# Kernel tuning notes

Hardware: AMD Instinct MI355X
Metric: run time of the kernel (lower is better)

## Reference

```python
import jax, jax.numpy as jnp
import numpy as np

B, S, D, H = 4, 2048, 1024, 4
HD = D // H


def setup_inputs() -> dict:
    key = jax.random.key(0)
    ks = jax.random.split(key, 6)
    s = 0.02  # init scale for projection weights
    return {
        "hidden_states": jax.random.normal(ks[0], (B, S, D), jnp.float32),
        "Wq": jax.random.normal(ks[1], (D, D), jnp.float32) * s,
        "Wk": jax.random.normal(ks[2], (D, D), jnp.float32) * s,
        "Wv": jax.random.normal(ks[3], (D, D), jnp.float32) * s,
        "Wo": jax.random.normal(ks[4], (D, D), jnp.float32) * s,
        "bo": jnp.zeros((D,), jnp.float32),
        "betas": jax.random.normal(ks[5], (1, H, 1, 1), jnp.float32),
        "mem": jnp.zeros((H, HD, HD), jnp.float32),
        "z": jnp.zeros((H, HD, 1), jnp.float32),
    }


def reference(hidden_states, Wq, Wk, Wv, Wo, bo, betas, mem, z):
    b, s, d = hidden_states.shape
    h = betas.shape[1]
    hd = d // h

    def split(x):  # [b,s,d] -> [b,h,s,hd]
        return x.reshape(b, s, h, hd).transpose(0, 2, 1, 3)

    q = split(hidden_states @ Wq.T)
    k = split(hidden_states @ Wk.T)
    v = split(hidden_states @ Wv.T)

    # standard causal attention (note: no 1/sqrt(d) scaling, faithful to source)
    aw = jnp.einsum('bhqd,bhkd->bhqk', q, k)
    causal = jnp.tril(jnp.ones((s, s), bool))
    aw = jnp.where(causal, aw, jnp.finfo(aw.dtype).min)
    p = jax.nn.softmax(aw, axis=-1)
    attn = jnp.einsum('bhqk,bhkd->bhqd', p, v)

    # linear-attention memory read
    sq = jax.nn.elu(q) + 1.0
    sk = jax.nn.elu(k) + 1.0
    A_mem = jnp.einsum('bhsd,hde->bhse', sq, mem) / (
        jnp.einsum('bhsd,hdo->bhso', sq, z) + 1e-6)

    # sigmoid-gated blend
    g = jax.nn.sigmoid(betas)
    out = g * A_mem + (1.0 - g) * attn

    # memory / z state update (delta rule), averaged over batch
    delta = jnp.einsum('bhsd,hde->bhse', sk, mem) / (
        jnp.einsum('bhsd,hdo->bhso', sk, z) + 1e-6)
    mem_new = mem + jnp.einsum('bhsd,bhse->hde', sk, v - delta) / b
    z_new = z + jnp.mean(jnp.sum(sk, axis=2), axis=0)[:, :, None]

    # merge heads + output projection
    out = out.transpose(0, 2, 1, 3).reshape(b, s, d)
    out = out @ Wo.T + bo
    return (out, mem_new, z_new)
```

## Files before the change

kernel.cpp:

```cpp
#include <hip/hip_runtime.h>

#define Bsz 4
#define Ssz 2048
#define Dsz 1024
#define Hsz 4
#define HDsz 256
#define Msz 8192

typedef unsigned short u16;
typedef __attribute__((ext_vector_type(8))) short bf16x8;
typedef __attribute__((ext_vector_type(4))) float f32x4;

__device__ __forceinline__ u16 f2b(float f) {
  unsigned u = __float_as_uint(f);
  return (u16)((u + 0x7FFFu + ((u >> 16) & 1u)) >> 16);
}
__device__ __forceinline__ unsigned pk2(float a, float b) {
  return (unsigned)f2b(a) | ((unsigned)f2b(b) << 16);
}

typedef const unsigned int __attribute__((address_space(1)))* gcp;
typedef unsigned int __attribute__((address_space(3)))* lcp;
__device__ __forceinline__ void gld16(const u16* g, u16* l) {
  __builtin_amdgcn_global_load_lds((gcp)g, (lcp)l, 16, 0, 0);
}

__global__ __launch_bounds__(256) void cvt_bf16(const float4* __restrict__ in,
                                                u16* __restrict__ outp) {
  size_t i = (size_t)blockIdx.x * 256 + threadIdx.x;
  float4 v = in[i];
  uint2 r; r.x = pk2(v.x, v.y); r.y = pk2(v.z, v.w);
  *(uint2*)(outp + i * 4) = r;
}

__global__ __launch_bounds__(256) void gemm_lds(const u16* __restrict__ A16,
                                                const u16* __restrict__ Wb,
                                                const float* __restrict__ bias,
                                                float* __restrict__ C32,
                                                u16* __restrict__ Cbf) {
  __shared__ u16 sA[128 * 32];
  __shared__ u16 sB[128 * 32];
  const int tid = threadIdx.x;
  const int lane = tid & 63, quad = lane >> 4, l15 = lane & 15;
  const int w = tid >> 6;
  const int mw = (w >> 1) * 64, nw = (w & 1) * 64;
  const int m0 = blockIdx.y * 128, n0 = blockIdx.x * 128;
  const int r0 = tid >> 2, seg = (tid & 3) * 8;
  const u16* ga0 = A16 + (size_t)(m0 + r0) * Dsz + seg;
  const u16* gb0 = Wb + (size_t)(n0 + r0) * Dsz + seg;
  u16* lA0 = sA + w * 512;
  u16* lA1 = sA + 2048 + w * 512;
  u16* lB0 = sB + w * 512;
  u16* lB1 = sB + 2048 + w * 512;
  f32x4 acc[4][4] = {};
  for (int k0 = 0; k0 < Dsz; k0 += 32) {
    __syncthreads();
    gld16(ga0 + k0, lA0);
    gld16(ga0 + (size_t)64 * Dsz + k0, lA1);
    gld16(gb0 + k0, lB0);
    gld16(gb0 + (size_t)64 * Dsz + k0, lB1);
    __syncthreads();
    bf16x8 af[4], bfr[4];
#pragma unroll
    for (int i = 0; i < 4; ++i) {
      af[i] = *(const bf16x8*)&sA[(mw + i * 16 + l15) * 32 + quad * 8];
      bfr[i] = *(const bf16x8*)&sB[(nw + i * 16 + l15) * 32 + quad * 8];
    }
#pragma unroll
    for (int i = 0; i < 4; ++i)
#pragma unroll
      for (int j = 0; j < 4; ++j)
        acc[i][j] = __builtin_amdgcn_mfma_f32_16x16x32_bf16(af[i], bfr[j], acc[i][j], 0, 0, 0);
  }
#pragma unroll
  for (int j = 0; j < 4; ++j) {
    const int n = n0 + nw + j * 16 + l15;
    const float bv = bias ? bias[n] : 0.f;
#pragma unroll
    for (int i = 0; i < 4; ++i) {
#pragma unroll
      for (int r = 0; r < 4; ++r) {
        const int m = m0 + mw + i * 16 + quad * 4 + r;
        const float val = acc[i][j][r] + bv;
        const size_t idx = (size_t)m * Dsz + n;
        if (C32) C32[idx] = val;
        if (Cbf) Cbf[idx] = f2b(val);
      }
    }
  }
}

__global__ __launch_bounds__(256) void transpose_v(const float* __restrict__ V,
                                                   u16* __restrict__ Vt) {
  __shared__ u16 tile[32 * 36];
  const int t = threadIdx.x;
  const int s0 = blockIdx.x * 32, e0 = blockIdx.y * 32, bh = blockIdx.z;
  const int b = bh >> 2, h = bh & 3;
  {
    const int s_l = t >> 3, e8 = (t & 7) * 4;
    float4 v = *(const float4*)(V + ((size_t)(b * Ssz) + s0 + s_l) * Dsz + h * HDsz + e0 + e8);
    uint2 r; r.x = pk2(v.x, v.y); r.y = pk2(v.z, v.w);
    *(uint2*)&tile[s_l * 36 + e8] = r;
  }
  __syncthreads();
  {
    const int e_l = t >> 3, s4 = (t & 7) * 4;
    u16 a = tile[(s4 + 0) * 36 + e_l], b2 = tile[(s4 + 1) * 36 + e_l];
    u16 c = tile[(s4 + 2) * 36 + e_l], d = tile[(s4 + 3) * 36 + e_l];
    uint2 r; r.x = (unsigned)a | ((unsigned)b2 << 16);
    r.y = (unsigned)c | ((unsigned)d << 16);
    *(uint2*)(Vt + ((size_t)bh * HDsz + e0 + e_l) * Ssz + s0 + s4) = r;
  }
}

__global__ __launch_bounds__(256, 2) void attn_mfma(const u16* __restrict__ Qg,
                                                    const u16* __restrict__ Kg,
                                                    const u16* __restrict__ Vtg,
                                                    float* __restrict__ At,
                                                    float* __restrict__ Pb,
                                                    float* __restrict__ mlb) {
  const int x = blockIdx.x;
  int qt, cc; bool split;
  if (x < 40) { qt = 31 - (x >> 1); cc = x & 1; split = true; }
  else { qt = 51 - x; cc = 0; split = false; }
  const int bh = blockIdx.y, b = bh >> 2, h = bh & 3;
  const int tid = threadIdx.x, w = tid >> 6, lane = tid & 63;
  const int quad = lane >> 4, l15 = lane & 15;
  __shared__ u16 sK[2][32 * 256];
  __shared__ u16 sV[2][256 * 32];
  const int q0w = qt * 64 + w * 16;
  bf16x8 qf[8];
  {
    const u16* qp = Qg + ((size_t)(b * Ssz) + q0w + l15) * Dsz + h * HDsz + quad * 8;
#pragma unroll
    for (int dd = 0; dd < 8; ++dd) qf[dd] = *(const bf16x8*)(qp + dd * 32);
  }
  f32x4 o[16] = {};
  float m_old = -1e30f, l = 0.f;
  const int nkt = 2 * qt + 2, half = qt + 1;
  const int kt_lo = (split && cc) ? half : 0;
  const int kt_hi = (split && !cc) ? half : nkt;
  const u16* kstage = Kg + ((size_t)(b * Ssz) + (tid >> 5)) * Dsz + h * HDsz
                      + (((tid & 31) ^ ((tid >> 5) & 7)) << 3);
  const u16* vstage = Vtg + ((size_t)bh * HDsz + (tid >> 2)) * Ssz
                      + (((tid & 3) ^ ((tid >> 3) & 3)) << 3);
  int bufc = 0;
  {
    const u16* kp = kstage + (size_t)(kt_lo * 32) * Dsz;
    const u16* vp = vstage + kt_lo * 32;
#pragma unroll
    for (int i = 0; i < 4; ++i) {
      gld16(kp + (size_t)i * 8 * Dsz, &sK[0][w * 512 + i * 2048]);
      gld16(vp + (size_t)i * 64 * Ssz, &sV[0][w * 512 + i * 2048]);
    }
  }
  for (int kt = kt_lo; kt < kt_hi; ++kt) {
    const int j0 = kt * 32;
    __syncthreads();
    if (kt + 1 < kt_hi) {
      const u16* kp = kstage + (size_t)((kt + 1) * 32) * Dsz;
      const u16* vp = vstage + (kt + 1) * 32;
      const int bn = bufc ^ 1;
#pragma unroll
      for (int i = 0; i < 4; ++i) {
        gld16(kp + (size_t)i * 8 * Dsz, &sK[bn][w * 512 + i * 2048]);
        gld16(vp + (size_t)i * 64 * Ssz, &sV[bn][w * 512 + i * 2048]);
      }
    }
    f32x4 s0v = {}, s1v = {};
#pragma unroll
    for (int dd = 0; dd < 8; ++dd) {
      const int c0 = ((dd * 4 + quad) ^ (l15 & 7)) << 3;
      bf16x8 a0 = *(const bf16x8*)&sK[bufc][l15 * 256 + c0];
      bf16x8 a1 = *(const bf16x8*)&sK[bufc][(16 + l15) * 256 + c0];
      s0v = __builtin_amdgcn_mfma_f32_16x16x32_bf16(a0, qf[dd], s0v, 0, 0, 0);
      s1v = __builtin_amdgcn_mfma_f32_16x16x32_bf16(a1, qf[dd], s1v, 0, 0, 0);
    }
    const int qg = q0w + l15;
    float p[8];
#pragma unroll
    for (int r = 0; r < 4; ++r) {
      const int kg = j0 + quad * 4 + r;
      p[r] = (kg <= qg) ? s0v[r] : -1e30f;
      p[4 + r] = (kg + 16 <= qg) ? s1v[r] : -1e30f;
    }
    float mt = p[0];
#pragma unroll
    for (int i = 1; i < 8; ++i) mt = fmaxf(mt, p[i]);
    mt = fmaxf(mt, __shfl_xor(mt, 16));
    mt = fmaxf(mt, __shfl_xor(mt, 32));
    const float m_new = fmaxf(m_old, mt);
    const float alpha = __expf(m_old - m_new);
    float ts = 0.f;
#pragma unroll
    for (int i = 0; i < 8; ++i) { p[i] = __expf(p[i] - m_new); ts += p[i]; }
    ts += __shfl_xor(ts, 16);
    ts += __shfl_xor(ts, 32);
    l = l * alpha + ts;
    m_old = m_new;
    if (!__all(alpha == 1.0f)) {
      const float a0_ = __shfl(alpha, (lane & 48) | (quad * 4 + 0));
      const float a1_ = __shfl(alpha, (lane & 48) | (quad * 4 + 1));
      const float a2_ = __shfl(alpha, (lane & 48) | (quad * 4 + 2));
      const float a3_ = __shfl(alpha, (lane & 48) | (quad * 4 + 3));
#pragma unroll
      for (int ds = 0; ds < 16; ++ds) {
        o[ds][0] *= a0_; o[ds][1] *= a1_; o[ds][2] *= a2_; o[ds][3] *= a3_;
      }
    }
    float xx[8];
#pragma unroll
    for (int i = 0; i < 8; ++i) xx[i] = __shfl_xor(p[i], 16);
    const bool qe = (quad & 1) == 0;
    float Alo[8], Ahi[8];
#pragma unroll
    for (int i = 0; i < 4; ++i) {
      Alo[i] = qe ? p[i] : xx[i];
      Alo[4 + i] = qe ? xx[i] : p[i];
      Ahi[i] = qe ? p[4 + i] : xx[4 + i];
      Ahi[4 + i] = qe ? xx[4 + i] : p[4 + i];
    }
    float zz[8];
    const bool sendlo = (quad & 1) != 0;
#pragma unroll
    for (int i = 0; i < 8; ++i) zz[i] = __shfl_xor(sendlo ? Alo[i] : Ahi[i], 32);
    float fin[8];
#pragma unroll
    for (int i = 0; i < 8; ++i)
      fin[i] = (quad == 0) ? Alo[i] : (quad == 3) ? Ahi[i] : zz[i];
    uint4 pkv;
    pkv.x = pk2(fin[0], fin[1]); pkv.y = pk2(fin[2], fin[3]);
    pkv.z = pk2(fin[4], fin[5]); pkv.w = pk2(fin[6], fin[7]);
    bf16x8 pf = *(bf16x8*)&pkv;
    const int vc0 = (quad ^ ((l15 >> 1) & 3)) << 3;
#pragma unroll
    for (int ds = 0; ds < 16; ++ds) {
      bf16x8 bv = *(const bf16x8*)&sV[bufc][(ds * 16 + l15) * 32 + vc0];
      o[ds] = __builtin_amdgcn_mfma_f32_16x16x32_bf16(pf, bv, o[ds], 0, 0, 0);
    }
    bufc ^= 1;
  }
  if (!split) {
    float lr[4];
#pragma unroll
    for (int r = 0; r < 4; ++r) lr[r] = 1.f / __shfl(l, (lane & 48) | (quad * 4 + r));
    float* ob = At + ((size_t)bh * Ssz + q0w + quad * 4) * HDsz + l15;
#pragma unroll
    for (int r = 0; r < 4; ++r)
#pragma unroll
      for (int ds = 0; ds < 16; ++ds)
        ob[(size_t)r * HDsz + ds * 16] = o[ds][r] * lr[r];
  } else {
    float* dst;
    if (cc == 0)
      dst = At + ((size_t)bh * Ssz + q0w + quad * 4) * HDsz + l15;
    else
      dst = Pb + ((size_t)((bh * 20 + (qt - 12)) * 64) + w * 16 + quad * 4) * HDsz + l15;
#pragma unroll
    for (int r = 0; r < 4; ++r)
#pragma unroll
      for (int ds = 0; ds < 16; ++ds)
        dst[(size_t)r * HDsz + ds * 16] = o[ds][r];
    if (lane < 16) {
      const int idx = (bh * 20 + (qt - 12)) * 64 + w * 16 + l15;
      mlb[cc * 40960 + idx] = m_old;
      mlb[cc * 40960 + 20480 + idx] = l;
    }
  }
}

__global__ __launch_bounds__(256) void attn_merge(float* __restrict__ At,
                                                  const float* __restrict__ Pb,
                                                  const float* __restrict__ mlb) {
  const int qx = blockIdx.x, bh = blockIdx.y;
  const int t = threadIdx.x;
  const int slot = (bh * 20 + qx) * 64;
  float4* abase = (float4*)(At + ((size_t)bh * Ssz + (12 + qx) * 64) * HDsz);
  const float4* pbase = (const float4*)(Pb + (size_t)slot * HDsz);
#pragma unroll
  for (int i = 0; i < 16; ++i) {
    const int f = i * 256 + t;
    const int qr = f >> 6;
    const int idx = slot + qr;
    const float m0 = mlb[idx], l0 = mlb[20480 + idx];
    const float m1 = mlb[40960 + idx], l1 = mlb[61440 + idx];
    const float mm = fmaxf(m0, m1);
    const float w0 = __expf(m0 - mm), w1 = __expf(m1 - mm);
    const float inv = 1.f / (l0 * w0 + l1 * w1);
    float4 av = abase[f];
    float4 pv = pbase[f];
    float4 ov;
    ov.x = (av.x * w0 + pv.x * w1) * inv;
    ov.y = (av.y * w0 + pv.y * w1) * inv;
    ov.z = (av.z * w0 + pv.z * w1) * inv;
    ov.w = (av.w * w0 + pv.w * w1) * inv;
    abase[f] = ov;
  }
}

__global__ __launch_bounds__(256) void eludens(float* __restrict__ Qb,
                                               float* __restrict__ Kb,
                                               const float* __restrict__ z,
                                               float* __restrict__ dq,
                                               float* __restrict__ dk) {
  const int wid = threadIdx.x >> 6, lane = threadIdx.x & 63;
  const int r = blockIdx.x * 4 + wid;
  const int b = r >> 13, h = (r >> 11) & 3, s = r & 2047;
  const size_t base = ((size_t)(b * Ssz + s)) * Dsz + h * HDsz + lane * 4;
  float4 z4 = *(const float4*)(z + h * HDsz + lane * 4);
  float4 q = *(float4*)(Qb + base);
  q.x = q.x > 0.f ? q.x + 1.f : __expf(q.x);
  q.y = q.y > 0.f ? q.y + 1.f : __expf(q.y);
  q.z = q.z > 0.f ? q.z + 1.f : __expf(q.z);
  q.w = q.w > 0.f ? q.w + 1.f : __expf(q.w);
  *(float4*)(Qb + base) = q;
  float4 k = *(float4*)(Kb + base);
  k.x = k.x > 0.f ? k.x + 1.f : __expf(k.x);
  k.y = k.y > 0.f ? k.y + 1.f : __expf(k.y);
  k.z = k.z > 0.f ? k.z + 1.f : __expf(k.z);
  k.w = k.w > 0.f ? k.w + 1.f : __expf(k.w);
  *(float4*)(Kb + base) = k;
  float pq = q.x * z4.x + q.y * z4.y + q.z * z4.z + q.w * z4.w;
  float pk = k.x * z4.x + k.y * z4.y + k.z * z4.z + k.w * z4.w;
#pragma unroll
  for (int off = 32; off; off >>= 1) {
    pq += __shfl_down(pq, off);
    pk += __shfl_down(pk, off);
  }
  if (lane == 0) { dq[r] = pq; dk[r] = pk; }
}

__global__ __launch_bounds__(256) void memread_mfma(const float* __restrict__ Asrc,
                                                    const float* __restrict__ mem,
                                                    const float* __restrict__ dens,
                                                    const float* __restrict__ betas,
                                                    const float* __restrict__ At,
                                                    float* __restrict__ Vio,
                                                    u16* __restrict__ bfout, int mode) {
  const int h = blockIdx.z;
  const int tid = threadIdx.x, lane = tid & 63, w = tid >> 6;
  const int quad = lane >> 4, l15 = lane & 15;
  const int mw = (w >> 1) * 64, ew = (w & 1) * 64;
  const int m0 = blockIdx.y * 128, e0t = blockIdx.x * 128;
  __shared__ u16 sA[128 * 40];
  __shared__ u16 sB[128 * 40];
  const int srow = tid >> 1, sseg = (tid & 1) * 16;
  const int k4 = (tid & 7) * 4, e4 = (tid >> 3) * 4;
  f32x4 acc[4][4] = {};
  for (int k0 = 0; k0 < HDsz; k0 += 32) {
    __syncthreads();
    {
      const float* ap = Asrc + (size_t)(m0 + srow) * Dsz + h * HDsz + k0 + sseg;
      float4 f0 = *(const float4*)ap, f1 = *(const float4*)(ap + 4);
      float4 f2 = *(const float4*)(ap + 8), f3 = *(const float4*)(ap + 12);
      uint4 u0, u1;
      u0.x = pk2(f0.x, f0.y); u0.y = pk2(f0.z, f0.w);
      u0.z = pk2(f1.x, f1.y); u0.w = pk2(f1.z, f1.w);
      u1.x = pk2(f2.x, f2.y); u1.y = pk2(f2.z, f2.w);
      u1.z = pk2(f3.x, f3.y); u1.w = pk2(f3.z, f3.w);
      u16* dst = &sA[srow * 40 + sseg];
      *(uint4*)dst = u0; *(uint4*)(dst + 8) = u1;
    }
    {
      const float* bp = mem + (size_t)h * 65536 + (size_t)(k0 + k4) * HDsz + e0t + e4;
      float4 r0 = *(const float4*)bp;
      float4 r1 = *(const float4*)(bp + HDsz);
      float4 r2 = *(const float4*)(bp + 2 * HDsz);
      float4 r3 = *(const float4*)(bp + 3 * HDsz);
      const float* rr[4] = {(const float*)&r0, (const float*)&r1,
                            (const float*)&r2, (const float*)&r3};
#pragma unroll
      for (int c = 0; c < 4; ++c) {
        uint2 u;
        u.x = pk2(rr[0][c], rr[1][c]);
        u.y = pk2(rr[2][c], rr[3][c]);
        *(uint2*)&sB[(e4 + c) * 40 + k4] = u;
      }
    }
    __syncthreads();
    bf16x8 af[4], bfr[4];
#pragma unroll
    for (int i = 0; i < 4; ++i) {
      af[i] = *(const bf16x8*)&sA[(mw + i * 16 + l15) * 40 + quad * 8];
      bfr[i] = *(const bf16x8*)&sB[(ew + i * 16 + l15) * 40 + quad * 8];
    }
#pragma unroll
    for (int i = 0; i < 4; ++i)
#pragma unroll
      for (int j = 0; j < 4; ++j)
        acc[i][j] = __builtin_amdgcn_mfma_f32_16x16x32_bf16(af[i], bfr[j], acc[i][j], 0, 0, 0);
  }
  const float g = 1.f / (1.f + __expf(-betas[h]));
#pragma unroll
  for (int i = 0; i < 4; ++i) {
#pragma unroll
    for (int r = 0; r < 4; ++r) {
      const int m = m0 + mw + i * 16 + quad * 4 + r;
      const int b = m >> 11, s = m & 2047;
      const int rowidx = ((b << 2) + h) * Ssz + s;
      const float inv = 1.f / (dens[rowidx] + 1e-6f);
#pragma unroll
      for (int j = 0; j < 4; ++j) {
        const int e = e0t + ew + j * 16 + l15;
        const float av = acc[i][j][r] * inv;
        if (mode == 0) {
          const float a = At[(size_t)rowidx * HDsz + e];
          bfout[(size_t)m * Dsz + h * HDsz + e] = f2b(g * av + (1.f - g) * a);
        } else {
          float* p = Vio + (size_t)m * Dsz + h * HDsz + e;
          *p = *p - av;
        }
      }
    }
  }
}

__global__ __launch_bounds__(256) void mem_update_mfma(const float* __restrict__ SK,
                                                       const float* __restrict__ W,
                                                       float* __restrict__ P) {
  const int de = blockIdx.x;
  const int d0 = (de >> 1) * 128, e0 = (de & 1) * 128;
  const int h = blockIdx.y, chunk = blockIdx.z;
  const int m0 = chunk * 512;
  const int tid = threadIdx.x, lane = tid & 63, w = tid >> 6;
  const int quad = lane >> 4, l15 = lane & 15;
  const int dw = (w >> 1) * 64, ew = (w & 1) * 64;
  __shared__ u16 sA[128 * 40];
  __shared__ u16 sB[128 * 40];
  const int m4 = (tid & 7) * 4;
  const int c4 = (tid >> 3) * 4;
  f32x4 acc[4][4] = {};
  for (int mt = 0; mt < 512; mt += 32) {
    __syncthreads();
    const float* ka = SK + (size_t)(m0 + mt + m4) * Dsz + h * HDsz + d0 + c4;
    const float* wa = W + (size_t)(m0 + mt + m4) * Dsz + h * HDsz + e0 + c4;
    float4 a0 = *(const float4*)ka;
    float4 a1 = *(const float4*)(ka + Dsz);
    float4 a2 = *(const float4*)(ka + 2 * Dsz);
    float4 a3 = *(const float4*)(ka + 3 * Dsz);
    float4 b0 = *(const float4*)wa;
    float4 b1 = *(const float4*)(wa + Dsz);
    float4 b2 = *(const float4*)(wa + 2 * Dsz);
    float4 b3 = *(const float4*)(wa + 3 * Dsz);
    const float* aa[4] = {(const float*)&a0, (const float*)&a1,
                          (const float*)&a2, (const float*)&a3};
    const float* bb[4] = {(const float*)&b0, (const float*)&b1,
                          (const float*)&b2, (const float*)&b3};
#pragma unroll
    for (int c = 0; c < 4; ++c) {
      uint2 ua, ub2;
      ua.x = pk2(aa[0][c], aa[1][c]); ua.y = pk2(aa[2][c], aa[3][c]);
      ub2.x = pk2(bb[0][c], bb[1][c]); ub2.y = pk2(bb[2][c], bb[3][c]);
      *(uint2*)&sA[(c4 + c) * 40 + m4] = ua;
      *(uint2*)&sB[(c4 + c) * 40 + m4] = ub2;
    }
    __syncthreads();
    bf16x8 af[4], bfr[4];
#pragma unroll
    for (int i = 0; i < 4; ++i) {
      af[i] = *(const bf16x8*)&sA[(dw + i * 16 + l15) * 40 + quad * 8];
      bfr[i] = *(const bf16x8*)&sB[(ew + i * 16 + l15) * 40 + quad * 8];
    }
#pragma unroll
    for (int i = 0; i < 4; ++i)
#pragma unroll
      for (int j = 0; j < 4; ++j)
        acc[i][j] = __builtin_amdgcn_mfma_f32_16x16x32_bf16(af[i], bfr[j], acc[i][j], 0, 0, 0);
  }
  float* Pp = P + ((size_t)(h * 16 + chunk)) * 65536;
#pragma unroll
  for (int i = 0; i < 4; ++i)
#pragma unroll
    for (int r = 0; r < 4; ++r) {
      const int d = d0 + dw + i * 16 + quad * 4 + r;
#pragma unroll
      for (int j = 0; j < 4; ++j) {
        const int e = e0 + ew + j * 16 + l15;
        Pp[(size_t)d * HDsz + e] = acc[i][j][r];
      }
    }
}

__global__ __launch_bounds__(256) void mem_reduce(const float4* __restrict__ P,
                                                  const float4* __restrict__ mem,
                                                  float4* __restrict__ outmem) {
  const int gid = blockIdx.x * 256 + threadIdx.x;
  const int h = gid >> 14, off = gid & 16383;
  float sx = 0.f, sy = 0.f, sz = 0.f, sw = 0.f;
#pragma unroll 4
  for (int c = 0; c < 16; ++c) {
    float4 v = P[((size_t)(h * 16 + c) << 14) + off];
    sx += v.x; sy += v.y; sz += v.z; sw += v.w;
  }
  float4 m = mem[gid];
  float4 o;
  o.x = m.x + 0.25f * sx; o.y = m.y + 0.25f * sy;
  o.z = m.z + 0.25f * sz; o.w = m.w + 0.25f * sw;
  outmem[gid] = o;
}

__global__ __launch_bounds__(256) void z_update(const float* __restrict__ SK,
                                                const float* __restrict__ z_in,
                                                float* __restrict__ z_out) {
  const int h = blockIdx.x >> 4, chunk = blockIdx.x & 15;
  const int t = threadIdx.x;
  const int m0 = chunk * 512;
  float sum = 0.f;
  for (int i = 0; i < 512; ++i) sum += SK[(size_t)(m0 + i) * Dsz + h * HDsz + t];
  float val = sum * 0.25f;
  if (chunk == 0) val += z_in[h * HDsz + t];
  atomicAdd(z_out + h * HDsz + t, val);
}

extern "C" void kernel_launch(void* const* d_in, const int* in_sizes, int n_in,
                              void* d_out, int out_size, void* d_ws, size_t ws_size,
                              hipStream_t stream) {
  (void)in_sizes; (void)n_in; (void)out_size; (void)ws_size;
  const float* Hs = (const float*)d_in[0];
  const float* Wq = (const float*)d_in[1];
  const float* Wk = (const float*)d_in[2];
  const float* Wv = (const float*)d_in[3];
  const float* Wo = (const float*)d_in[4];
  const float* bo = (const float*)d_in[5];
  const float* betas = (const float*)d_in[6];
  const float* mem = (const float*)d_in[7];
  const float* z = (const float*)d_in[8];

  float* ws = (float*)d_ws;
  float* Qb = ws;
  float* Kb = ws + 8388608;
  float* Vb = ws + 16777216;
  float* At = ws + 25165824;
  float* dq = ws + 33554432;
  float* dk = ws + 33587200;
  float* mlb = ws + 33619968;
  u16* ub = (u16*)(ws + 33701888);
  u16* Wqb = ub;
  u16* Wkb = ub + 1048576;
  u16* Wvb = ub + 2097152;
  u16* Wob = ub + 3145728;
  u16* Qbf = ub + 4194304;
  u16* Kbf = ub + 12582912;
  u16* Vt = ub + 20971520;
  u16* Hsb = Vt;
  float* P = (float*)Vt;
  float* Pb = (float*)d_out;

  float* out = (float*)d_out;
  float* outmem = out + (size_t)Msz * Dsz;
  float* outz = outmem + Hsz * HDsz * HDsz;

  hipMemsetAsync(outz, 0, (size_t)(Hsz * HDsz) * sizeof(float), stream);

  cvt_bf16<<<1024, 256, 0, stream>>>((const float4*)Wq, Wqb);
  cvt_bf16<<<1024, 256, 0, stream>>>((const float4*)Wk, Wkb);
  cvt_bf16<<<1024, 256, 0, stream>>>((const float4*)Wv, Wvb);
  cvt_bf16<<<1024, 256, 0, stream>>>((const float4*)Wo, Wob);
  cvt_bf16<<<8192, 256, 0, stream>>>((const float4*)Hs, Hsb);

  dim3 gg(8, 64);
  gemm_lds<<<gg, 256, 0, stream>>>(Hsb, Wqb, nullptr, Qb, Qbf);
  gemm_lds<<<gg, 256, 0, stream>>>(Hsb, Wkb, nullptr, Kb, Kbf);
  gemm_lds<<<gg, 256, 0, stream>>>(Hsb, Wvb, nullptr, Vb, nullptr);

  transpose_v<<<dim3(64, 8, 16), 256, 0, stream>>>(Vb, Vt);
  attn_mfma<<<dim3(52, 16), 256, 0, stream>>>(Qbf, Kbf, Vt, At, Pb, mlb);
  attn_merge<<<dim3(20, 16), 256, 0, stream>>>(At, Pb, mlb);

  eludens<<<8192, 256, 0, stream>>>(Qb, Kb, z, dq, dk);

  memread_mfma<<<dim3(2, 64, 4), 256, 0, stream>>>(Qb, mem, dq, betas, At, nullptr, Qbf, 0);
  memread_mfma<<<dim3(2, 64, 4), 256, 0, stream>>>(Kb, mem, dk, betas, nullptr, Vb, nullptr, 1);

  mem_update_mfma<<<dim3(4, 4, 16), 256, 0, stream>>>(Kb, Vb, P);
  mem_reduce<<<256, 256, 0, stream>>>((const float4*)P, (const float4*)mem, (float4*)outmem);
  z_update<<<64, 256, 0, stream>>>(Kb, z, outz);

  gemm_lds<<<gg, 256, 0, stream>>>(Qbf, Wob, bo, out, nullptr);
}
```

Baseline: 542.4 us.

## Double-buffer GEMM LDS, rebalance attention with 128-row tiles, parallelize z_update

The projection GEMM now double-buffers its LDS tiles, prefetching the next K slice while MFMAs run on the current one, and drops one barrier per iteration. Causal attention moves to 512-thread blocks covering 128 query rows, scheduled from a static table that splits long rows into up to three KV chunks for load balance. The merge kernel is extended to combine three partial softmax states. z_update spreads its reduction over many more blocks using float4 loads and an LDS reduction. Risks include higher register pressure at 512 threads and more atomics.

```diff
diff --git a/kernel.cpp b/kernel.cpp
--- a/kernel.cpp
+++ b/kernel.cpp
@@ -38,8 +38,8 @@
                                                 const float* __restrict__ bias,
                                                 float* __restrict__ C32,
                                                 u16* __restrict__ Cbf) {
-  __shared__ u16 sA[128 * 32];
-  __shared__ u16 sB[128 * 32];
+  __shared__ u16 sA[2][128 * 32];
+  __shared__ u16 sB[2][128 * 32];
   const int tid = threadIdx.x;
   const int lane = tid & 63, quad = lane >> 4, l15 = lane & 15;
   const int w = tid >> 6;
@@ -48,29 +48,35 @@
   const int r0 = tid >> 2, seg = (tid & 3) * 8;
   const u16* ga0 = A16 + (size_t)(m0 + r0) * Dsz + seg;
   const u16* gb0 = Wb + (size_t)(n0 + r0) * Dsz + seg;
-  u16* lA0 = sA + w * 512;
-  u16* lA1 = sA + 2048 + w * 512;
-  u16* lB0 = sB + w * 512;
-  u16* lB1 = sB + 2048 + w * 512;
   f32x4 acc[4][4] = {};
+  {
+    gld16(ga0, &sA[0][w * 512]);
+    gld16(ga0 + (size_t)64 * Dsz, &sA[0][2048 + w * 512]);
+    gld16(gb0, &sB[0][w * 512]);
+    gld16(gb0 + (size_t)64 * Dsz, &sB[0][2048 + w * 512]);
+  }
+  int buf = 0;
   for (int k0 = 0; k0 < Dsz; k0 += 32) {
     __syncthreads();
-    gld16(ga0 + k0, lA0);
-    gld16(ga0 + (size_t)64 * Dsz + k0, lA1);
-    gld16(gb0 + k0, lB0);
-    gld16(gb0 + (size_t)64 * Dsz + k0, lB1);
-    __syncthreads();
+    if (k0 + 32 < Dsz) {
+      const int kn = k0 + 32, bn = buf ^ 1;
+      gld16(ga0 + kn, &sA[bn][w * 512]);
+      gld16(ga0 + (size_t)64 * Dsz + kn, &sA[bn][2048 + w * 512]);
+      gld16(gb0 + kn, &sB[bn][w * 512]);
+      gld16(gb0 + (size_t)64 * Dsz + kn, &sB[bn][2048 + w * 512]);
+    }
     bf16x8 af[4], bfr[4];
 #pragma unroll
     for (int i = 0; i < 4; ++i) {
-      af[i] = *(const bf16x8*)&sA[(mw + i * 16 + l15) * 32 + quad * 8];
-      bfr[i] = *(const bf16x8*)&sB[(nw + i * 16 + l15) * 32 + quad * 8];
+      af[i] = *(const bf16x8*)&sA[buf][(mw + i * 16 + l15) * 32 + quad * 8];
+      bfr[i] = *(const bf16x8*)&sB[buf][(nw + i * 16 + l15) * 32 + quad * 8];
     }
 #pragma unroll
     for (int i = 0; i < 4; ++i)
 #pragma unroll
       for (int j = 0; j < 4; ++j)
         acc[i][j] = __builtin_amdgcn_mfma_f32_16x16x32_bf16(af[i], bfr[j], acc[i][j], 0, 0, 0);
+    buf ^= 1;
   }
 #pragma unroll
   for (int j = 0; j < 4; ++j) {
@@ -113,22 +119,34 @@
   }
 }
 
-__global__ __launch_bounds__(256, 2) void attn_mfma(const u16* __restrict__ Qg,
+#define CH(qt, k, lo, hi) \
+  ((unsigned)(qt) | ((unsigned)(k) << 8) | ((unsigned)(lo) << 16) | ((unsigned)(hi) << 24))
+
+__global__ __launch_bounds__(512, 4) void attn_mfma(const u16* __restrict__ Qg,
                                                     const u16* __restrict__ Kg,
                                                     const u16* __restrict__ Vtg,
                                                     float* __restrict__ At,
                                                     float* __restrict__ Pb,
                                                     float* __restrict__ mlb) {
-  const int x = blockIdx.x;
-  int qt, cc; bool split;
-  if (x < 40) { qt = 31 - (x >> 1); cc = x & 1; split = true; }
-  else { qt = 51 - x; cc = 0; split = false; }
+  static const unsigned int tab[32] = {
+      CH(11, 0, 0, 24), CH(11, 1, 24, 48), CH(10, 0, 0, 22), CH(10, 1, 22, 44),
+      CH(15, 0, 0, 22), CH(15, 1, 22, 43), CH(15, 2, 43, 64), CH(9, 0, 0, 20),
+      CH(9, 1, 20, 40),  CH(14, 0, 0, 20), CH(14, 1, 20, 40), CH(14, 2, 40, 60),
+      CH(13, 0, 0, 19),  CH(13, 1, 19, 38), CH(13, 2, 38, 56), CH(8, 0, 0, 18),
+      CH(8, 1, 18, 36),  CH(12, 0, 0, 18), CH(12, 1, 18, 35), CH(12, 2, 35, 52),
+      CH(7, 0, 0, 16),   CH(7, 1, 16, 32), CH(3, 0, 0, 16),   CH(6, 0, 0, 14),
+      CH(6, 1, 14, 28),  CH(5, 0, 0, 12),  CH(5, 1, 12, 24),  CH(2, 0, 0, 12),
+      CH(4, 0, 0, 10),   CH(4, 1, 10, 20), CH(1, 0, 0, 8),    CH(0, 0, 0, 4)};
+  const unsigned int e = tab[blockIdx.x];
+  const int qt = e & 255, ck = (e >> 8) & 255;
+  const int kt_lo = (e >> 16) & 255, kt_hi = e >> 24;
+  const int nc = (qt < 4) ? 1 : ((qt < 12) ? 2 : 3);
   const int bh = blockIdx.y, b = bh >> 2, h = bh & 3;
   const int tid = threadIdx.x, w = tid >> 6, lane = tid & 63;
   const int quad = lane >> 4, l15 = lane & 15;
   __shared__ u16 sK[2][32 * 256];
   __shared__ u16 sV[2][256 * 32];
-  const int q0w = qt * 64 + w * 16;
+  const int q0w = qt * 128 + w * 16;
   bf16x8 qf[8];
   {
     const u16* qp = Qg + ((size_t)(b * Ssz) + q0w + l15) * Dsz + h * HDsz + quad * 8;
@@ -137,9 +155,6 @@
   }
   f32x4 o[16] = {};
   float m_old = -1e30f, l = 0.f;
-  const int nkt = 2 * qt + 2, half = qt + 1;
-  const int kt_lo = (split && cc) ? half : 0;
-  const int kt_hi = (split && !cc) ? half : nkt;
   const u16* kstage = Kg + ((size_t)(b * Ssz) + (tid >> 5)) * Dsz + h * HDsz
                       + (((tid & 31) ^ ((tid >> 5) & 7)) << 3);
   const u16* vstage = Vtg + ((size_t)bh * HDsz + (tid >> 2)) * Ssz
@@ -149,9 +164,9 @@
     const u16* kp = kstage + (size_t)(kt_lo * 32) * Dsz;
     const u16* vp = vstage + kt_lo * 32;
 #pragma unroll
-    for (int i = 0; i < 4; ++i) {
-      gld16(kp + (size_t)i * 8 * Dsz, &sK[0][w * 512 + i * 2048]);
-      gld16(vp + (size_t)i * 64 * Ssz, &sV[0][w * 512 + i * 2048]);
+    for (int i = 0; i < 2; ++i) {
+      gld16(kp + (size_t)i * 16 * Dsz, &sK[0][w * 512 + i * 4096]);
+      gld16(vp + (size_t)i * 128 * Ssz, &sV[0][w * 512 + i * 4096]);
     }
   }
   for (int kt = kt_lo; kt < kt_hi; ++kt) {
@@ -162,9 +177,9 @@
       const u16* vp = vstage + (kt + 1) * 32;
       const int bn = bufc ^ 1;
 #pragma unroll
-      for (int i = 0; i < 4; ++i) {
-        gld16(kp + (size_t)i * 8 * Dsz, &sK[bn][w * 512 + i * 2048]);
-        gld16(vp + (size_t)i * 64 * Ssz, &sV[bn][w * 512 + i * 2048]);
+      for (int i = 0; i < 2; ++i) {
+        gld16(kp + (size_t)i * 16 * Dsz, &sK[bn][w * 512 + i * 4096]);
+        gld16(vp + (size_t)i * 128 * Ssz, &sV[bn][w * 512 + i * 4096]);
       }
     }
     f32x4 s0v = {}, s1v = {};
@@ -240,7 +255,7 @@
     }
     bufc ^= 1;
   }
-  if (!split) {
+  if (nc == 1) {
     float lr[4];
 #pragma unroll
     for (int r = 0; r < 4; ++r) lr[r] = 1.f / __shfl(l, (lane & 48) | (quad * 4 + r));
@@ -252,19 +267,23 @@
         ob[(size_t)r * HDsz + ds * 16] = o[ds][r] * lr[r];
   } else {
     float* dst;
-    if (cc == 0)
+    if (ck == 0) {
       dst = At + ((size_t)bh * Ssz + q0w + quad * 4) * HDsz + l15;
-    else
-      dst = Pb + ((size_t)((bh * 20 + (qt - 12)) * 64) + w * 16 + quad * 4) * HDsz + l15;
+    } else {
+      const int sec = (qt < 12) ? (qt - 4) : (8 + (qt - 12) * 2 + (ck - 1));
+      dst = Pb + (size_t)(bh * 16 + sec) * 32768
+            + (size_t)(w * 16 + quad * 4) * HDsz + l15;
+    }
 #pragma unroll
     for (int r = 0; r < 4; ++r)
 #pragma unroll
       for (int ds = 0; ds < 16; ++ds)
         dst[(size_t)r * HDsz + ds * 16] = o[ds][r];
     if (lane < 16) {
-      const int idx = (bh * 20 + (qt - 12)) * 64 + w * 16 + l15;
-      mlb[cc * 40960 + idx] = m_old;
-      mlb[cc * 40960 + 20480 + idx] = l;
+      const int mlbase = ((bh * 12 + (qt - 4)) * 3 + ck) * 256;
+      const int mlrow = w * 16 + l15;
+      mlb[mlbase + mlrow] = m_old;
+      mlb[mlbase + 128 + mlrow] = l;
     }
   }
 }
@@ -272,28 +291,43 @@
 __global__ __launch_bounds__(256) void attn_merge(float* __restrict__ At,
                                                   const float* __restrict__ Pb,
                                                   const float* __restrict__ mlb) {
-  const int qx = blockIdx.x, bh = blockIdx.y;
+  const int qq = blockIdx.x, bh = blockIdx.y;
+  const int qt = qq + 4;
+  const int nc = (qt < 12) ? 2 : 3;
   const int t = threadIdx.x;
-  const int slot = (bh * 20 + qx) * 64;
-  float4* abase = (float4*)(At + ((size_t)bh * Ssz + (12 + qx) * 64) * HDsz);
-  const float4* pbase = (const float4*)(Pb + (size_t)slot * HDsz);
-#pragma unroll
-  for (int i = 0; i < 16; ++i) {
+  const int mlbase = (bh * 12 + qq) * 3 * 256;
+  const int sec1 = (qt < 12) ? (qt - 4) : (8 + (qt - 12) * 2);
+  float4* abase = (float4*)(At + ((size_t)bh * Ssz + (size_t)qt * 128) * HDsz);
+  const float4* p1 = (const float4*)(Pb + (size_t)(bh * 16 + sec1) * 32768);
+  const float4* p2 = p1 + 8192;
+#pragma unroll
+  for (int i = 0; i < 32; ++i) {
     const int f = i * 256 + t;
     const int qr = f >> 6;
-    const int idx = slot + qr;
-    const float m0 = mlb[idx], l0 = mlb[20480 + idx];
-    const float m1 = mlb[40960 + idx], l1 = mlb[61440 + idx];
-    const float mm = fmaxf(m0, m1);
+    const float m0 = mlb[mlbase + qr],       l0 = mlb[mlbase + 128 + qr];
+    const float m1 = mlb[mlbase + 256 + qr], l1 = mlb[mlbase + 384 + qr];
+    float mm = fmaxf(m0, m1);
+    float m2 = -1e30f, l2 = 0.f;
+    if (nc == 3) {
+      m2 = mlb[mlbase + 512 + qr]; l2 = mlb[mlbase + 640 + qr];
+      mm = fmaxf(mm, m2);
+    }
     const float w0 = __expf(m0 - mm), w1 = __expf(m1 - mm);
-    const float inv = 1.f / (l0 * w0 + l1 * w1);
+    const float w2 = (nc == 3) ? __expf(m2 - mm) : 0.f;
+    const float inv = 1.f / (l0 * w0 + l1 * w1 + l2 * w2);
     float4 av = abase[f];
-    float4 pv = pbase[f];
+    float4 pv = p1[f];
     float4 ov;
-    ov.x = (av.x * w0 + pv.x * w1) * inv;
-    ov.y = (av.y * w0 + pv.y * w1) * inv;
-    ov.z = (av.z * w0 + pv.z * w1) * inv;
-    ov.w = (av.w * w0 + pv.w * w1) * inv;
+    ov.x = av.x * w0 + pv.x * w1;
+    ov.y = av.y * w0 + pv.y * w1;
+    ov.z = av.z * w0 + pv.z * w1;
+    ov.w = av.w * w0 + pv.w * w1;
+    if (nc == 3) {
+      float4 qv = p2[f];
+      ov.x += qv.x * w2; ov.y += qv.y * w2;
+      ov.z += qv.z * w2; ov.w += qv.w * w2;
+    }
+    ov.x *= inv; ov.y *= inv; ov.z *= inv; ov.w *= inv;
     abase[f] = ov;
   }
 }
@@ -502,14 +536,35 @@
 __global__ __launch_bounds__(256) void z_update(const float* __restrict__ SK,
                                                 const float* __restrict__ z_in,
                                                 float* __restrict__ z_out) {
-  const int h = blockIdx.x >> 4, chunk = blockIdx.x & 15;
-  const int t = threadIdx.x;
-  const int m0 = chunk * 512;
-  float sum = 0.f;
-  for (int i = 0; i < 512; ++i) sum += SK[(size_t)(m0 + i) * Dsz + h * HDsz + t];
-  float val = sum * 0.25f;
-  if (chunk == 0) val += z_in[h * HDsz + t];
-  atomicAdd(z_out + h * HDsz + t, val);
+  __shared__ float4 red[256];
+  const int h = blockIdx.x >> 7, chunk = blockIdx.x & 127;
+  const int wid = threadIdx.x >> 6, lane = threadIdx.x & 63;
+  const int m0 = chunk * 64;
+  float4 s = {0.f, 0.f, 0.f, 0.f};
+#pragma unroll
+  for (int i = 0; i < 16; ++i) {
+    const int row = m0 + i * 4 + wid;
+    float4 v = *(const float4*)(SK + (size_t)row * Dsz + h * HDsz + lane * 4);
+    s.x += v.x; s.y += v.y; s.z += v.z; s.w += v.w;
+  }
+  red[wid * 64 + lane] = s;
+  __syncthreads();
+  if (wid == 0) {
+    float4 a = red[lane], b = red[64 + lane], c = red[128 + lane], d = red[192 + lane];
+    a.x = (a.x + b.x + c.x + d.x) * 0.25f;
+    a.y = (a.y + b.y + c.y + d.y) * 0.25f;
+    a.z = (a.z + b.z + c.z + d.z) * 0.25f;
+    a.w = (a.w + b.w + c.w + d.w) * 0.25f;
+    if (chunk == 0) {
+      const float4 z4 = *(const float4*)(z_in + h * HDsz + lane * 4);
+      a.x += z4.x; a.y += z4.y; a.z += z4.z; a.w += z4.w;
+    }
+    float* zp = z_out + h * HDsz + lane * 4;
+    atomicAdd(zp + 0, a.x);
+    atomicAdd(zp + 1, a.y);
+    atomicAdd(zp + 2, a.z);
+    atomicAdd(zp + 3, a.w);
+  }
 }
 
 extern "C" void kernel_launch(void* const* d_in, const int* in_sizes, int n_in,
@@ -534,7 +589,7 @@
   float* dq = ws + 33554432;
   float* dk = ws + 33587200;
   float* mlb = ws + 33619968;
-  u16* ub = (u16*)(ws + 33701888);
+  u16* ub = (u16*)(ws + 33767424);
   u16* Wqb = ub;
   u16* Wkb = ub + 1048576;
   u16* Wvb = ub + 2097152;
@@ -564,8 +619,8 @@
   gemm_lds<<<gg, 256, 0, stream>>>(Hsb, Wvb, nullptr, Vb, nullptr);
 
   transpose_v<<<dim3(64, 8, 16), 256, 0, stream>>>(Vb, Vt);
-  attn_mfma<<<dim3(52, 16), 256, 0, stream>>>(Qbf, Kbf, Vt, At, Pb, mlb);
-  attn_merge<<<dim3(20, 16), 256, 0, stream>>>(At, Pb, mlb);
+  attn_mfma<<<dim3(32, 16), 512, 0, stream>>>(Qbf, Kbf, Vt, At, Pb, mlb);
+  attn_merge<<<dim3(12, 16), 256, 0, stream>>>(At, Pb, mlb);
 
   eludens<<<8192, 256, 0, stream>>>(Qb, Kb, z, dq, dk);
 
@@ -574,7 +629,7 @@
 
   mem_update_mfma<<<dim3(4, 4, 16), 256, 0, stream>>>(Kb, Vb, P);
   mem_reduce<<<256, 256, 0, stream>>>((const float4*)P, (const float4*)mem, (float4*)outmem);
-  z_update<<<64, 256, 0, stream>>>(Kb, z, outz);
+  z_update<<<512, 256, 0, stream>>>(Kb, z, outz);
 
   gemm_lds<<<gg, 256, 0, stream>>>(Qbf, Wob, bo, out, nullptr);
 }
```

Result: slower. 685.9 us (+26.5%).

## Reorder attention block schedule, raise MFMA priority, parallelize z reduction

Applied to the files above, without the earlier changes.

The attention kernel now takes its (query tile, split half) assignment from a lookup table that interleaves the short unsplit tiles among the long split ones, aiming for better load balance. It also drops the min-blocks-per-CU launch bound and wraps the MFMA loops in s_setprio so matrix work gets issue priority. Separately, z_update is rewritten to use 512 blocks with float4 loads and an LDS reduction across waves, replacing 64 blocks that each ran a 512-row serial loop. The trade-offs are possible register and occupancy changes from the new launch bounds, and more atomic adds on z.

```diff
diff --git a/kernel.cpp b/kernel.cpp
--- a/kernel.cpp
+++ b/kernel.cpp
@@ -113,16 +113,43 @@
   }
 }
 
-__global__ __launch_bounds__(256, 2) void attn_mfma(const u16* __restrict__ Qg,
-                                                    const u16* __restrict__ Kg,
-                                                    const u16* __restrict__ Vtg,
-                                                    float* __restrict__ At,
-                                                    float* __restrict__ Pb,
-                                                    float* __restrict__ mlb) {
-  const int x = blockIdx.x;
-  int qt, cc; bool split;
-  if (x < 40) { qt = 31 - (x >> 1); cc = x & 1; split = true; }
-  else { qt = 51 - x; cc = 0; split = false; }
+__global__ __launch_bounds__(256) void attn_mfma(const u16* __restrict__ Qg,
+                                                 const u16* __restrict__ Kg,
+                                                 const u16* __restrict__ Vtg,
+                                                 float* __restrict__ At,
+                                                 float* __restrict__ Pb,
+                                                 float* __restrict__ mlb) {
+  static const unsigned char tab[52] = {
+      (unsigned char)(31|0x80), (unsigned char)(31|0xC0),
+      (unsigned char)(30|0x80), (unsigned char)(30|0xC0),
+      (unsigned char)(29|0x80), (unsigned char)(29|0xC0),
+      (unsigned char)(28|0x80), (unsigned char)(28|0xC0),
+      (unsigned char)(27|0x80), (unsigned char)(27|0xC0),
+      (unsigned char)(26|0x80), (unsigned char)(26|0xC0),
+      (unsigned char)(25|0x80), (unsigned char)(25|0xC0),
+      (unsigned char)(24|0x80), (unsigned char)(24|0xC0),
+      (unsigned char)(23|0x80), (unsigned char)(23|0xC0),
+      11,
+      (unsigned char)(22|0x80), (unsigned char)(22|0xC0),
+      (unsigned char)(21|0x80), (unsigned char)(21|0xC0),
+      10,
+      (unsigned char)(20|0x80), (unsigned char)(20|0xC0),
+      (unsigned char)(19|0x80), (unsigned char)(19|0xC0),
+      9,
+      (unsigned char)(18|0x80), (unsigned char)(18|0xC0),
+      (unsigned char)(17|0x80), (unsigned char)(17|0xC0),
+      8,
+      (unsigned char)(16|0x80), (unsigned char)(16|0xC0),
+      (unsigned char)(15|0x80), (unsigned char)(15|0xC0),
+      7,
+      (unsigned char)(14|0x80), (unsigned char)(14|0xC0),
+      (unsigned char)(13|0x80), (unsigned char)(13|0xC0),
+      6,
+      (unsigned char)(12|0x80), (unsigned char)(12|0xC0),
+      5, 4, 3, 2, 1, 0};
+  const int e = tab[blockIdx.x];
+  const int qt = e & 63, cc = (e >> 6) & 1;
+  const bool split = (e >> 7) != 0;
   const int bh = blockIdx.y, b = bh >> 2, h = bh & 3;
   const int tid = threadIdx.x, w = tid >> 6, lane = tid & 63;
   const int quad = lane >> 4, l15 = lane & 15;
@@ -168,6 +195,7 @@
       }
     }
     f32x4 s0v = {}, s1v = {};
+    __builtin_amdgcn_s_setprio(1);
 #pragma unroll
     for (int dd = 0; dd < 8; ++dd) {
       const int c0 = ((dd * 4 + quad) ^ (l15 & 7)) << 3;
@@ -176,6 +204,7 @@
       s0v = __builtin_amdgcn_mfma_f32_16x16x32_bf16(a0, qf[dd], s0v, 0, 0, 0);
       s1v = __builtin_amdgcn_mfma_f32_16x16x32_bf16(a1, qf[dd], s1v, 0, 0, 0);
     }
+    __builtin_amdgcn_s_setprio(0);
     const int qg = q0w + l15;
     float p[8];
 #pragma unroll
@@ -233,11 +262,13 @@
     pkv.z = pk2(fin[4], fin[5]); pkv.w = pk2(fin[6], fin[7]);
     bf16x8 pf = *(bf16x8*)&pkv;
     const int vc0 = (quad ^ ((l15 >> 1) & 3)) << 3;
+    __builtin_amdgcn_s_setprio(1);
 #pragma unroll
     for (int ds = 0; ds < 16; ++ds) {
       bf16x8 bv = *(const bf16x8*)&sV[bufc][(ds * 16 + l15) * 32 + vc0];
       o[ds] = __builtin_amdgcn_mfma_f32_16x16x32_bf16(pf, bv, o[ds], 0, 0, 0);
     }
+    __builtin_amdgcn_s_setprio(0);
     bufc ^= 1;
   }
   if (!split) {
@@ -502,14 +533,35 @@
 __global__ __launch_bounds__(256) void z_update(const float* __restrict__ SK,
                                                 const float* __restrict__ z_in,
                                                 float* __restrict__ z_out) {
-  const int h = blockIdx.x >> 4, chunk = blockIdx.x & 15;
-  const int t = threadIdx.x;
-  const int m0 = chunk * 512;
-  float sum = 0.f;
-  for (int i = 0; i < 512; ++i) sum += SK[(size_t)(m0 + i) * Dsz + h * HDsz + t];
-  float val = sum * 0.25f;
-  if (chunk == 0) val += z_in[h * HDsz + t];
-  atomicAdd(z_out + h * HDsz + t, val);
+  __shared__ float4 red[256];
+  const int h = blockIdx.x >> 7, chunk = blockIdx.x & 127;
+  const int wid = threadIdx.x >> 6, lane = threadIdx.x & 63;
+  const int m0 = chunk * 64;
+  float4 s = {0.f, 0.f, 0.f, 0.f};
+#pragma unroll
+  for (int i = 0; i < 16; ++i) {
+    const int row = m0 + i * 4 + wid;
+    float4 v = *(const float4*)(SK + (size_t)row * Dsz + h * HDsz + lane * 4);
+    s.x += v.x; s.y += v.y; s.z += v.z; s.w += v.w;
+  }
+  red[wid * 64 + lane] = s;
+  __syncthreads();
+  if (wid == 0) {
+    float4 a = red[lane], b = red[64 + lane], c = red[128 + lane], d = red[192 + lane];
+    a.x = (a.x + b.x + c.x + d.x) * 0.25f;
+    a.y = (a.y + b.y + c.y + d.y) * 0.25f;
+    a.z = (a.z + b.z + c.z + d.z) * 0.25f;
+    a.w = (a.w + b.w + c.w + d.w) * 0.25f;
+    if (chunk == 0) {
+      const float4 z4 = *(const float4*)(z_in + h * HDsz + lane * 4);
+      a.x += z4.x; a.y += z4.y; a.z += z4.z; a.w += z4.w;
+    }
+    float* zp = z_out + h * HDsz + lane * 4;
+    atomicAdd(zp + 0, a.x);
+    atomicAdd(zp + 1, a.y);
+    atomicAdd(zp + 2, a.z);
+    atomicAdd(zp + 3, a.w);
+  }
 }
 
 extern "C" void kernel_launch(void* const* d_in, const int* in_sizes, int n_in,
@@ -574,7 +626,7 @@
 
   mem_update_mfma<<<dim3(4, 4, 16), 256, 0, stream>>>(Kb, Vb, P);
   mem_reduce<<<256, 256, 0, stream>>>((const float4*)P, (const float4*)mem, (float4*)outmem);
-  z_update<<<64, 256, 0, stream>>>(Kb, z, outz);
+  z_update<<<512, 256, 0, stream>>>(Kb, z, outz);
 
   gemm_lds<<<gg, 256, 0, stream>>>(Qbf, Wob, bo, out, nullptr);
 }
```

Measured after the change: 554.5 us. +2.2%, slower.
